# Kernel optimization log

Hardware: AMD Instinct MI355X
Metric: run time of the kernel (lower is better)

The kernel has to match this reference:

```python
import jax, jax.numpy as jnp
import numpy as np

B, R, S, D, K = 4096, 49, 50, 512, 100

def setup_inputs() -> dict:
    key = jax.random.key(0)
    ks = jax.random.split(key, 10)
    return {
        "ifeature": jax.random.normal(ks[0], (B, R, D), dtype=jnp.float32),
        "tfeature_h": jax.random.normal(ks[1], (B, S, D), dtype=jnp.float32),
        "w_Vi_0": jax.random.normal(ks[2], (D, K), dtype=jnp.float32) * 0.05,
        "w_Vt_0": jax.random.normal(ks[3], (D, K), dtype=jnp.float32) * 0.05,
        "w_Pi_0": jax.random.normal(ks[4], (2 * K, 1), dtype=jnp.float32) * 0.05,
        "b_Pi_0": jnp.zeros((R,), dtype=jnp.float32),
        "w_Vi_1": jax.random.normal(ks[5], (D, K), dtype=jnp.float32) * 0.05,
        "w_Vt_1": jax.random.normal(ks[6], (D, K), dtype=jnp.float32) * 0.05,
        "w_Pi_1": jax.random.normal(ks[7], (2 * K, 1), dtype=jnp.float32) * 0.05,
        "b_Pi_1": jnp.zeros((S,), dtype=jnp.float32),
    }

def reference(ifeature, tfeature_h, w_Vi_0, w_Vt_0, w_Pi_0, b_Pi_0,
              w_Vi_1, w_Vt_1, w_Pi_1, b_Pi_1):
    # ---- pass 0: attend over image regions, conditioned on mean text feature
    tfeature = jnp.mean(tfeature_h, axis=1)                      # [B, D]
    wVi0 = jnp.einsum('brd,dk->brk', ifeature, w_Vi_0)           # [B, R, K]
    wVt0 = (tfeature @ w_Vt_0)[:, None, :]                       # [B, 1, K] -> broadcast over R
    Hi = jnp.tanh(jnp.concatenate(
        [wVi0, jnp.broadcast_to(wVt0, wVi0.shape)], axis=-1))    # [B, R, 2K]
    scores_i = jnp.squeeze(Hi @ w_Pi_0, axis=-1) + b_Pi_0        # [B, R]
    Pi = jax.nn.softmax(scores_i, axis=-1)                       # [B, R]
    Vi = jnp.einsum('br,brd->bd', Pi, ifeature)                  # [B, D]
    # ---- pass 1: attend over text positions, conditioned on attended image
    wVi1 = (Vi @ w_Vi_1)[:, None, :]                             # [B, 1, K]
    wVt1 = jnp.einsum('bsd,dk->bsk', tfeature_h, w_Vt_1)         # [B, S, K]
    Ht = jnp.tanh(jnp.concatenate(
        [jnp.broadcast_to(wVi1, wVt1.shape), wVt1], axis=-1))    # [B, S, 2K]
    scores_t = jnp.squeeze(Ht @ w_Pi_1, axis=-1) + b_Pi_1        # [B, S]
    Pt = jax.nn.softmax(scores_t, axis=-1)                       # [B, S]
    Vt = jnp.einsum('bs,bsd->bd', Pt, tfeature_h)                # [B, D]
    return Vi + Vt
```

## Files before the change

kernel.cpp:

```cpp
#include <hip/hip_runtime.h>
#include <math.h>

#define NB 4096
#define NR 49
#define NS 50
#define ND 512
#define NK 100
#define NT 7
#define KSTEPS 16
#define FRAGS (NT * KSTEPS * 64 * 8)

typedef __attribute__((ext_vector_type(8))) short short8;
typedef __attribute__((ext_vector_type(4))) float f32x4;

__device__ __forceinline__ unsigned short f32_bf16(float f) {
    union { float f; unsigned u; } x; x.f = f;
    return (unsigned short)((x.u + 0x7fffu + ((x.u >> 16) & 1u)) >> 16);
}
__device__ __forceinline__ float bf16_f32(unsigned short h) {
    union { unsigned u; float f; } x; x.u = ((unsigned)h) << 16;
    return x.f;
}
__device__ __forceinline__ unsigned cvt_pk_bf16(float lo, float hi) {
    unsigned r;
    asm("v_cvt_pk_bf16_f32 %0, %1, %2" : "=v"(r) : "v"(lo), "v"(hi));
    return r;
}
__device__ __forceinline__ float fast_tanh(float x) {
    const float ax = fabsf(x);
    const float e = __expf(2.f * ax);
    const float r = 1.f - 2.f / (e + 1.f);
    return copysignf(r, x);
}

__global__ void preswz_kernel(const float* __restrict__ w0, const float* __restrict__ w1,
                              unsigned short* __restrict__ ws)
{
    const int l  = threadIdx.x;
    const int gk = blockIdx.x & 15;
    const int t  = blockIdx.x >> 4;
    const int m  = blockIdx.y;
    const float* W = m ? w1 : w0;
    const int col = t * 16 + (l & 15);
    const int k0  = gk * 32 + (l >> 4) * 8;
    unsigned short* o = ws + (size_t)m * FRAGS + ((size_t)(t * 16 + gk) * 64 + l) * 8;
#pragma unroll
    for (int j = 0; j < 8; ++j) {
        float v = (col < NK) ? W[(size_t)(k0 + j) * NK + col] : 0.f;
        o[j] = f32_bf16(v);
    }
}

struct SM {
    short buf[NS * ND];
    float part[NT][64];
    float P[64];
};

__global__ __launch_bounds__(512, 6) void coattn_main(
    const float* __restrict__ ifeat, const float* __restrict__ tfeat,
    const float* __restrict__ wPi0, const float* __restrict__ bPi0,
    const float* __restrict__ wPi1, const float* __restrict__ bPi1,
    const unsigned short* __restrict__ wsW, float* __restrict__ out)
{
    __shared__ SM sm;
    const int b = blockIdx.x, tid = threadIdx.x;
    const int lane = tid & 63, wid = tid >> 6;
    const int colg = lane & 15, g = lane >> 4;
    const int wch = tid >> 3, wlo = tid & 7;

    float vi = 0.f;

    for (int pass = 0; pass < 2; ++pass) {
        const float* feat = pass ? (tfeat + (size_t)b * NS * ND)
                                 : (ifeat + (size_t)b * NR * ND);
        const int nrows  = pass ? NS : NR;
        const int nclamp = nrows - 1;
        const unsigned short* wsR = wsW + (size_t)pass * FRAGS;
        const float* wPiRow = pass ? (wPi1 + NK) : wPi0;
        const float* bvec   = pass ? bPi1 : bPi0;

        const int nitems = nrows * 64;
        for (int it = tid; it < nitems; it += 512) {
            const int r = it >> 6, c = it & 63;
            const float* p = feat + (r << 9) + (c << 3);
            const float4 a  = *reinterpret_cast<const float4*>(p);
            const float4 b4 = *reinterpret_cast<const float4*>(p + 4);
            uint4 v;
            v.x = cvt_pk_bf16(a.x, a.y);   v.y = cvt_pk_bf16(a.z, a.w);
            v.z = cvt_pk_bf16(b4.x, b4.y); v.w = cvt_pk_bf16(b4.z, b4.w);
            *reinterpret_cast<uint4*>(&sm.buf[(r << 9) + ((c ^ (r & 7)) << 3)]) = v;
        }
        __syncthreads();

        if (wid < NT) {
            int arow_[4], rswz_[4];
#pragma unroll
            for (int rt = 0; rt < 4; ++rt) {
                const int r0 = rt * 16 + colg;
                arow_[rt] = (r0 < nclamp) ? r0 : nclamp;
                rswz_[rt] = arow_[rt] & 7;
            }
            const f32x4 zero4 = {0.f, 0.f, 0.f, 0.f};
            f32x4 acc[4] = {zero4, zero4, zero4, zero4};
            const unsigned short* wl = wsR + ((size_t)wid * KSTEPS * 64 + lane) * 8;
#pragma unroll
            for (int ks = 0; ks < KSTEPS; ++ks) {
                const short8 w = *reinterpret_cast<const short8*>(wl + ks * 512);
                const int q0 = (ks << 2) + g;
#pragma unroll
                for (int rt = 0; rt < 4; ++rt) {
                    const short8 a = *reinterpret_cast<const short8*>(
                        &sm.buf[(arow_[rt] << 9) + ((q0 ^ rswz_[rt]) << 3)]);
                    acc[rt] = __builtin_amdgcn_mfma_f32_16x16x32_bf16(a, w, acc[rt], 0, 0, 0);
                }
            }

            const int col = wid * 16 + colg;
            const float w = (col < NK) ? wPiRow[col] : 0.f;
            float sp[4][4];
#pragma unroll
            for (int rt = 0; rt < 4; ++rt)
#pragma unroll
                for (int i = 0; i < 4; ++i)
                    sp[rt][i] = fast_tanh(acc[rt][i]) * w;
#pragma unroll
            for (int off = 1; off < 16; off <<= 1)
#pragma unroll
                for (int rt = 0; rt < 4; ++rt)
#pragma unroll
                    for (int i = 0; i < 4; ++i)
                        sp[rt][i] += __shfl_xor(sp[rt][i], off);
            if (colg == 0) {
#pragma unroll
                for (int rt = 0; rt < 4; ++rt)
#pragma unroll
                    for (int i = 0; i < 4; ++i)
                        sm.part[wid][rt * 16 + g * 4 + i] = sp[rt][i];
            }
        }
        __syncthreads();

        if (tid < 64) {
            float v = (tid < nrows) ? bvec[tid] : 0.f;
#pragma unroll
            for (int w = 0; w < NT; ++w) v += sm.part[w][tid];
            v = (tid < nrows) ? v : -3.0e38f;
            float mx = v;
#pragma unroll
            for (int off = 32; off; off >>= 1) mx = fmaxf(mx, __shfl_xor(mx, off));
            const float e = (tid < nrows) ? __expf(v - mx) : 0.f;
            float su = e;
#pragma unroll
            for (int off = 32; off; off >>= 1) su += __shfl_xor(su, off);
            sm.P[tid] = e / su;
        }
        __syncthreads();

        {
            float v = 0.f;
            for (int r = 0; r < nrows; ++r) {
                const unsigned short u = (unsigned short)
                    sm.buf[(r << 9) + ((wch ^ (r & 7)) << 3) + wlo];
                v += sm.P[r] * bf16_f32(u);
            }
            if (pass == 0) vi = v;
            else out[(size_t)b * ND + tid] = vi + v;
        }
        __syncthreads();
    }
}

extern "C" void kernel_launch(void* const* d_in, const int* in_sizes, int n_in,
                              void* d_out, int out_size, void* d_ws, size_t ws_size,
                              hipStream_t stream) {
    const float* ifeat = (const float*)d_in[0];
    const float* tfeat = (const float*)d_in[1];
    const float* wVi0  = (const float*)d_in[2];
    const float* wPi0  = (const float*)d_in[4];
    const float* bPi0  = (const float*)d_in[5];
    const float* wVt1  = (const float*)d_in[7];
    const float* wPi1  = (const float*)d_in[8];
    const float* bPi1  = (const float*)d_in[9];
    float* outp = (float*)d_out;
    unsigned short* wsW = (unsigned short*)d_ws;

    hipLaunchKernelGGL(preswz_kernel, dim3(NT * KSTEPS, 2), dim3(64), 0, stream,
                       wVi0, wVt1, wsW);
    hipLaunchKernelGGL(coattn_main, dim3(NB), dim3(512), 0, stream,
                       ifeat, tfeat, wPi0, bPi0, wPi1, bPi1, wsW, outp);
}
```

Before: 316.4 us.

## Prefetch text features into registers during image pass to overlap loads

Unrolls the two-pass loop and issues the global loads and bf16 conversion of the text features into registers right after the image-pass MFMA. Those loads are then in flight during the tanh/softmax/weighted-sum stages of the image pass, and the values are written to shared memory once the buffer is free. This targets exposed global-load latency between passes. It costs 28 extra VGPRs per thread, so launch bounds are lowered from 6 to 4 blocks per CU, which reduces occupancy.

```diff
diff --git a/kernel.cpp b/kernel.cpp
--- a/kernel.cpp
+++ b/kernel.cpp
@@ -57,7 +57,7 @@
     float P[64];
 };
 
-__global__ __launch_bounds__(512, 6) void coattn_main(
+__global__ __launch_bounds__(512, 4) void coattn_main(
     const float* __restrict__ ifeat, const float* __restrict__ tfeat,
     const float* __restrict__ wPi0, const float* __restrict__ bPi0,
     const float* __restrict__ wPi1, const float* __restrict__ bPi1,
@@ -69,41 +69,40 @@
     const int colg = lane & 15, g = lane >> 4;
     const int wch = tid >> 3, wlo = tid & 7;
 
-    float vi = 0.f;
-
-    for (int pass = 0; pass < 2; ++pass) {
-        const float* feat = pass ? (tfeat + (size_t)b * NS * ND)
-                                 : (ifeat + (size_t)b * NR * ND);
-        const int nrows  = pass ? NS : NR;
-        const int nclamp = nrows - 1;
-        const unsigned short* wsR = wsW + (size_t)pass * FRAGS;
-        const float* wPiRow = pass ? (wPi1 + NK) : wPi0;
-        const float* bvec   = pass ? bPi1 : bPi0;
-
-        const int nitems = nrows * 64;
-        for (int it = tid; it < nitems; it += 512) {
-            const int r = it >> 6, c = it & 63;
-            const float* p = feat + (r << 9) + (c << 3);
-            const float4 a  = *reinterpret_cast<const float4*>(p);
-            const float4 b4 = *reinterpret_cast<const float4*>(p + 4);
-            uint4 v;
-            v.x = cvt_pk_bf16(a.x, a.y);   v.y = cvt_pk_bf16(a.z, a.w);
-            v.z = cvt_pk_bf16(b4.x, b4.y); v.w = cvt_pk_bf16(b4.z, b4.w);
-            *reinterpret_cast<uint4*>(&sm.buf[(r << 9) + ((c ^ (r & 7)) << 3)]) = v;
-        }
-        __syncthreads();
-
+    const float* ig = ifeat + (size_t)b * NR * ND;
+    const float* tg = tfeat + (size_t)b * NS * ND;
+
+    const f32x4 zero4 = {0.f, 0.f, 0.f, 0.f};
+
+#define STG_ITEM(SRC, U, GUARD)                                                   \
+    {                                                                             \
+        const int it = tid + ((U) << 9);                                          \
+        if (GUARD) {                                                              \
+            const int r = it >> 6, c = it & 63;                                   \
+            const float* p = (SRC) + (r << 9) + (c << 3);                         \
+            const float4 a  = *reinterpret_cast<const float4*>(p);                \
+            const float4 b4 = *reinterpret_cast<const float4*>(p + 4);            \
+            uint4 v;                                                              \
+            v.x = cvt_pk_bf16(a.x, a.y);   v.y = cvt_pk_bf16(a.z, a.w);           \
+            v.z = cvt_pk_bf16(b4.x, b4.y); v.w = cvt_pk_bf16(b4.z, b4.w);         \
+            *reinterpret_cast<uint4*>(&sm.buf[(r << 9) + ((c ^ (r & 7)) << 3)]) = v; \
+        }                                                                         \
+    }
+    STG_ITEM(ig, 0, true) STG_ITEM(ig, 1, true) STG_ITEM(ig, 2, true) STG_ITEM(ig, 3, true)
+    STG_ITEM(ig, 4, true) STG_ITEM(ig, 5, true) STG_ITEM(ig, 6, tid < 64)
+    __syncthreads();
+
+    f32x4 acc[4] = {zero4, zero4, zero4, zero4};
+    {
+        int arow_[4], rswz_[4];
+#pragma unroll
+        for (int rt = 0; rt < 4; ++rt) {
+            const int r0 = rt * 16 + colg;
+            arow_[rt] = (r0 < NR - 1) ? r0 : (NR - 1);
+            rswz_[rt] = arow_[rt] & 7;
+        }
         if (wid < NT) {
-            int arow_[4], rswz_[4];
-#pragma unroll
-            for (int rt = 0; rt < 4; ++rt) {
-                const int r0 = rt * 16 + colg;
-                arow_[rt] = (r0 < nclamp) ? r0 : nclamp;
-                rswz_[rt] = arow_[rt] & 7;
-            }
-            const f32x4 zero4 = {0.f, 0.f, 0.f, 0.f};
-            f32x4 acc[4] = {zero4, zero4, zero4, zero4};
-            const unsigned short* wl = wsR + ((size_t)wid * KSTEPS * 64 + lane) * 8;
+            const unsigned short* wl = wsW + ((size_t)wid * KSTEPS * 64 + lane) * 8;
 #pragma unroll
             for (int ks = 0; ks < KSTEPS; ++ks) {
                 const short8 w = *reinterpret_cast<const short8*>(wl + ks * 512);
@@ -115,60 +114,162 @@
                     acc[rt] = __builtin_amdgcn_mfma_f32_16x16x32_bf16(a, w, acc[rt], 0, 0, 0);
                 }
             }
-
-            const int col = wid * 16 + colg;
-            const float w = (col < NK) ? wPiRow[col] : 0.f;
-            float sp[4][4];
-#pragma unroll
-            for (int rt = 0; rt < 4; ++rt)
-#pragma unroll
-                for (int i = 0; i < 4; ++i)
-                    sp[rt][i] = fast_tanh(acc[rt][i]) * w;
-#pragma unroll
-            for (int off = 1; off < 16; off <<= 1)
-#pragma unroll
-                for (int rt = 0; rt < 4; ++rt)
-#pragma unroll
-                    for (int i = 0; i < 4; ++i)
-                        sp[rt][i] += __shfl_xor(sp[rt][i], off);
-            if (colg == 0) {
-#pragma unroll
-                for (int rt = 0; rt < 4; ++rt)
-#pragma unroll
-                    for (int i = 0; i < 4; ++i)
-                        sm.part[wid][rt * 16 + g * 4 + i] = sp[rt][i];
+        }
+    }
+
+    uint4 tr[7];
+#pragma unroll
+    for (int u = 0; u < 7; ++u) {
+        const int it = tid + (u << 9);
+        if (u < 6 || tid < 128) {
+            const int r = it >> 6, c = it & 63;
+            const float* p = tg + (r << 9) + (c << 3);
+            const float4 a  = *reinterpret_cast<const float4*>(p);
+            const float4 b4 = *reinterpret_cast<const float4*>(p + 4);
+            tr[u].x = cvt_pk_bf16(a.x, a.y);   tr[u].y = cvt_pk_bf16(a.z, a.w);
+            tr[u].z = cvt_pk_bf16(b4.x, b4.y); tr[u].w = cvt_pk_bf16(b4.z, b4.w);
+        }
+    }
+
+    if (wid < NT) {
+        const int col = wid * 16 + colg;
+        const float w = (col < NK) ? wPi0[col] : 0.f;
+        float sp[4][4];
+#pragma unroll
+        for (int rt = 0; rt < 4; ++rt)
+#pragma unroll
+            for (int i = 0; i < 4; ++i)
+                sp[rt][i] = fast_tanh(acc[rt][i]) * w;
+#pragma unroll
+        for (int off = 1; off < 16; off <<= 1)
+#pragma unroll
+            for (int rt = 0; rt < 4; ++rt)
+#pragma unroll
+                for (int i = 0; i < 4; ++i)
+                    sp[rt][i] += __shfl_xor(sp[rt][i], off);
+        if (colg == 0) {
+#pragma unroll
+            for (int rt = 0; rt < 4; ++rt)
+#pragma unroll
+                for (int i = 0; i < 4; ++i)
+                    sm.part[wid][rt * 16 + g * 4 + i] = sp[rt][i];
+        }
+    }
+    __syncthreads();
+
+    if (tid < 64) {
+        float v = (tid < NR) ? bPi0[tid] : 0.f;
+#pragma unroll
+        for (int w = 0; w < NT; ++w) v += sm.part[w][tid];
+        v = (tid < NR) ? v : -3.0e38f;
+        float mx = v;
+#pragma unroll
+        for (int off = 32; off; off >>= 1) mx = fmaxf(mx, __shfl_xor(mx, off));
+        const float e = (tid < NR) ? __expf(v - mx) : 0.f;
+        float su = e;
+#pragma unroll
+        for (int off = 32; off; off >>= 1) su += __shfl_xor(su, off);
+        sm.P[tid] = e / su;
+    }
+    __syncthreads();
+
+    float vi = 0.f;
+    for (int r = 0; r < NR; ++r) {
+        const unsigned short u = (unsigned short)
+            sm.buf[(r << 9) + ((wch ^ (r & 7)) << 3) + wlo];
+        vi += sm.P[r] * bf16_f32(u);
+    }
+    __syncthreads();
+
+#pragma unroll
+    for (int u = 0; u < 7; ++u) {
+        const int it = tid + (u << 9);
+        if (u < 6 || tid < 128) {
+            const int r = it >> 6, c = it & 63;
+            *reinterpret_cast<uint4*>(&sm.buf[(r << 9) + ((c ^ (r & 7)) << 3)]) = tr[u];
+        }
+    }
+    __syncthreads();
+
+#pragma unroll
+    for (int rt = 0; rt < 4; ++rt) acc[rt] = zero4;
+    {
+        int arow_[4], rswz_[4];
+#pragma unroll
+        for (int rt = 0; rt < 4; ++rt) {
+            const int r0 = rt * 16 + colg;
+            arow_[rt] = (r0 < NS - 1) ? r0 : (NS - 1);
+            rswz_[rt] = arow_[rt] & 7;
+        }
+        if (wid < NT) {
+            const unsigned short* wl = wsW + (size_t)FRAGS
+                                     + ((size_t)wid * KSTEPS * 64 + lane) * 8;
+#pragma unroll
+            for (int ks = 0; ks < KSTEPS; ++ks) {
+                const short8 w = *reinterpret_cast<const short8*>(wl + ks * 512);
+                const int q0 = (ks << 2) + g;
+#pragma unroll
+                for (int rt = 0; rt < 4; ++rt) {
+                    const short8 a = *reinterpret_cast<const short8*>(
+                        &sm.buf[(arow_[rt] << 9) + ((q0 ^ rswz_[rt]) << 3)]);
+                    acc[rt] = __builtin_amdgcn_mfma_f32_16x16x32_bf16(a, w, acc[rt], 0, 0, 0);
+                }
             }
         }
-        __syncthreads();
-
-        if (tid < 64) {
-            float v = (tid < nrows) ? bvec[tid] : 0.f;
-#pragma unroll
-            for (int w = 0; w < NT; ++w) v += sm.part[w][tid];
-            v = (tid < nrows) ? v : -3.0e38f;
-            float mx = v;
-#pragma unroll
-            for (int off = 32; off; off >>= 1) mx = fmaxf(mx, __shfl_xor(mx, off));
-            const float e = (tid < nrows) ? __expf(v - mx) : 0.f;
-            float su = e;
-#pragma unroll
-            for (int off = 32; off; off >>= 1) su += __shfl_xor(su, off);
-            sm.P[tid] = e / su;
-        }
-        __syncthreads();
-
-        {
-            float v = 0.f;
-            for (int r = 0; r < nrows; ++r) {
-                const unsigned short u = (unsigned short)
-                    sm.buf[(r << 9) + ((wch ^ (r & 7)) << 3) + wlo];
-                v += sm.P[r] * bf16_f32(u);
-            }
-            if (pass == 0) vi = v;
-            else out[(size_t)b * ND + tid] = vi + v;
-        }
-        __syncthreads();
-    }
+    }
+
+    if (wid < NT) {
+        const int col = wid * 16 + colg;
+        const float w = (col < NK) ? wPi1[NK + col] : 0.f;
+        float sp[4][4];
+#pragma unroll
+        for (int rt = 0; rt < 4; ++rt)
+#pragma unroll
+            for (int i = 0; i < 4; ++i)
+                sp[rt][i] = fast_tanh(acc[rt][i]) * w;
+#pragma unroll
+        for (int off = 1; off < 16; off <<= 1)
+#pragma unroll
+            for (int rt = 0; rt < 4; ++rt)
+#pragma unroll
+                for (int i = 0; i < 4; ++i)
+                    sp[rt][i] += __shfl_xor(sp[rt][i], off);
+        if (colg == 0) {
+#pragma unroll
+            for (int rt = 0; rt < 4; ++rt)
+#pragma unroll
+                for (int i = 0; i < 4; ++i)
+                    sm.part[wid][rt * 16 + g * 4 + i] = sp[rt][i];
+        }
+    }
+    __syncthreads();
+
+    if (tid < 64) {
+        float v = (tid < NS) ? bPi1[tid] : 0.f;
+#pragma unroll
+        for (int w = 0; w < NT; ++w) v += sm.part[w][tid];
+        v = (tid < NS) ? v : -3.0e38f;
+        float mx = v;
+#pragma unroll
+        for (int off = 32; off; off >>= 1) mx = fmaxf(mx, __shfl_xor(mx, off));
+        const float e = (tid < NS) ? __expf(v - mx) : 0.f;
+        float su = e;
+#pragma unroll
+        for (int off = 32; off; off >>= 1) su += __shfl_xor(su, off);
+        sm.P[tid] = e / su;
+    }
+    __syncthreads();
+
+    {
+        float v = 0.f;
+        for (int r = 0; r < NS; ++r) {
+            const unsigned short u = (unsigned short)
+                sm.buf[(r << 9) + ((wch ^ (r & 7)) << 3) + wlo];
+            v += sm.P[r] * bf16_f32(u);
+        }
+        out[(size_t)b * ND + tid] = vi + v;
+    }
+#undef STG_ITEM
 }
 
 extern "C" void kernel_launch(void* const* d_in, const int* in_sizes, int n_in,
```

New measurement: 415.0 us. 31.2% more time.
